# Kernel optimization log

Hardware: AMD Instinct MI355X
Metric: run time of the kernel (lower is better)

## Reference

```python
import jax, jax.numpy as jnp
import numpy as np
import math

D = 1024
H = 16
FF = 4096
BS = 4
N = 1024
NEG_INF = -jnp.inf


def layer_norm(x, g, b, eps=1e-5):
    mu = jnp.mean(x, axis=-1, keepdims=True)
    var = jnp.var(x, axis=-1, keepdims=True)
    return (x - mu) * jax.lax.rsqrt(var + eps) * g + b


def mha(x, kv, Wq, Wk, Wv, g, b, causal):
    bs, n, d = x.shape
    n_kv = kv.shape[1]
    hd = d // H
    q = (x @ Wq).reshape(bs, n, H, hd)
    k = (kv @ Wk).reshape(bs, n_kv, H, hd)
    v = (kv @ Wv).reshape(bs, n_kv, H, hd)
    # scores scaled by 1/sqrt(model_dim) as in the original (not head_dim!)
    scores = jnp.einsum('bihd,bjhd->bhij', q, k) / math.sqrt(d)
    if causal:
        i = jnp.arange(n)[:, None]
        j = jnp.arange(n_kv)[None, :]
        scores = jnp.where(j <= i, scores, NEG_INF)
    probs = jax.nn.softmax(scores, axis=-1)
    ctx = jnp.einsum('bhij,bjhd->bihd', probs, v).reshape(bs, n, d)
    return layer_norm(ctx + x, g, b)


def setup_inputs() -> dict:
    key = jax.random.key(0)
    ks = jax.random.split(key, 20)
    s_attn = 1.0 / math.sqrt(D)
    s_ff1 = 1.0 / math.sqrt(D)
    s_ff2 = 1.0 / math.sqrt(FF)
    return {
        'x': jax.random.normal(ks[0], (BS, N, D), jnp.float32),
        'encoder_out': jax.random.normal(ks[1], (BS, N, D), jnp.float32),
        'Wq1': jax.random.normal(ks[2], (D, D), jnp.float32) * s_attn,
        'Wk1': jax.random.normal(ks[3], (D, D), jnp.float32) * s_attn,
        'Wv1': jax.random.normal(ks[4], (D, D), jnp.float32) * s_attn,
        'g1': jnp.ones((D,), jnp.float32), 'b1': jnp.zeros((D,), jnp.float32),
        'Wq2': jax.random.normal(ks[5], (D, D), jnp.float32) * s_attn,
        'Wk2': jax.random.normal(ks[6], (D, D), jnp.float32) * s_attn,
        'Wv2': jax.random.normal(ks[7], (D, D), jnp.float32) * s_attn,
        'g2': jnp.ones((D,), jnp.float32), 'b2': jnp.zeros((D,), jnp.float32),
        'W_ff1': jax.random.normal(ks[8], (D, FF), jnp.float32) * s_ff1,
        'b_ff1': jnp.zeros((FF,), jnp.float32),
        'W_ff2': jax.random.normal(ks[9], (FF, D), jnp.float32) * s_ff2,
        'b_ff2': jnp.zeros((D,), jnp.float32),
        'g3': jnp.ones((D,), jnp.float32), 'b3': jnp.zeros((D,), jnp.float32),
    }


def reference(x, encoder_out, Wq1, Wk1, Wv1, g1, b1, Wq2, Wk2, Wv2, g2, b2,
              W_ff1, b_ff1, W_ff2, b_ff2, g3, b3):
    # masked (causal) self-attention
    x = mha(x, x, Wq1, Wk1, Wv1, g1, b1, causal=True)
    # cross-attention over encoder output
    x = mha(x, encoder_out, Wq2, Wk2, Wv2, g2, b2, causal=False)
    # feedforward with exact GELU, residual, layernorm
    h = jax.nn.gelu(x @ W_ff1 + b_ff1, approximate=False)
    out = h @ W_ff2 + b_ff2
    return layer_norm(out + x, g3, b3)
```

## Files before the change

### kernel.cpp

```cpp
#include <hip/hip_runtime.h>

typedef unsigned short u16;
typedef short bf16x8 __attribute__((ext_vector_type(8)));
typedef float f32x4 __attribute__((ext_vector_type(4)));
typedef unsigned short u16x8 __attribute__((ext_vector_type(8)));
typedef unsigned short u16x4 __attribute__((ext_vector_type(4)));

__device__ __forceinline__ u16 f2bf(float f) {
  unsigned u = __builtin_bit_cast(unsigned, f);
  u += 0x7fffu + ((u >> 16) & 1u);
  return (u16)(u >> 16);
}
__device__ __forceinline__ float bf2f(u16 v) {
  return __builtin_bit_cast(float, (unsigned)v << 16);
}

__device__ __forceinline__ void gload_lds16(const void* g, void* l) {
  __builtin_amdgcn_global_load_lds(
      (const __attribute__((address_space(1))) unsigned int*)g,
      (__attribute__((address_space(3))) unsigned int*)l, 16, 0, 0);
}

__global__ __launch_bounds__(256) void cast2_bf16_kernel(const float* __restrict__ s0,
                                                         u16* __restrict__ d0,
                                                         const float* __restrict__ s1,
                                                         u16* __restrict__ d1) {
  const float* s = blockIdx.y ? s1 : s0;
  u16* d = blockIdx.y ? d1 : d0;
  const size_t i = (size_t)blockIdx.x * 256 + threadIdx.x;
  const float4 a = ((const float4*)s)[2 * i];
  const float4 b = ((const float4*)s)[2 * i + 1];
  u16x8 o;
  o[0] = f2bf(a.x); o[1] = f2bf(a.y); o[2] = f2bf(a.z); o[3] = f2bf(a.w);
  o[4] = f2bf(b.x); o[5] = f2bf(b.y); o[6] = f2bf(b.z); o[7] = f2bf(b.w);
  ((u16x8*)d)[i] = o;
}

__global__ __launch_bounds__(256) void pack_bt3_kernel(const float* __restrict__ W0,
                                                       const float* __restrict__ W1,
                                                       const float* __restrict__ W2,
                                                       u16* __restrict__ Bt,
                                                       int K, int N) {
  const float* W = blockIdx.z == 0 ? W0 : (blockIdx.z == 1 ? W1 : W2);
  u16* dst0 = Bt + (size_t)blockIdx.z * K * N;
  __shared__ u16 sh[64][72];
  const int n0 = blockIdx.x * 64, k0 = blockIdx.y * 64;
  const int t = threadIdx.x;
  {
    const int kloc = t >> 2, nc = (t & 3) * 16;
    const float* src = W + (size_t)(k0 + kloc) * N + n0 + nc;
#pragma unroll
    for (int i = 0; i < 16; ++i) sh[kloc][nc + i] = f2bf(src[i]);
  }
  __syncthreads();
  {
    const int nloc = t >> 2, kc = (t & 3) * 16;
    u16 tmp[16];
#pragma unroll
    for (int i = 0; i < 16; ++i) tmp[i] = sh[kc + i][nloc];
    u16* dst = dst0 + (size_t)(n0 + nloc) * K + k0 + kc;
    *(u16x8*)dst = *(const u16x8*)tmp;
    *(u16x8*)(dst + 8) = *(const u16x8*)(tmp + 8);
  }
}

__global__ __launch_bounds__(256) void pack_bt_kernel(const float* __restrict__ W,
                                                      u16* __restrict__ Bt,
                                                      int K, int N) {
  __shared__ u16 sh[64][72];
  const int n0 = blockIdx.x * 64, k0 = blockIdx.y * 64;
  const int t = threadIdx.x;
  {
    const int kloc = t >> 2, nc = (t & 3) * 16;
    const float* src = W + (size_t)(k0 + kloc) * N + n0 + nc;
#pragma unroll
    for (int i = 0; i < 16; ++i) sh[kloc][nc + i] = f2bf(src[i]);
  }
  __syncthreads();
  {
    const int nloc = t >> 2, kc = (t & 3) * 16;
    u16 tmp[16];
#pragma unroll
    for (int i = 0; i < 16; ++i) tmp[i] = sh[kc + i][nloc];
    u16* dst = Bt + (size_t)(n0 + nloc) * K + k0 + kc;
    *(u16x8*)dst = *(const u16x8*)tmp;
    *(u16x8*)(dst + 8) = *(const u16x8*)(tmp + 8);
  }
}

template <int EPI, int VOUT>
__global__ __launch_bounds__(512, 4) void gemm_bt(const u16* __restrict__ A,
                                                  const u16* __restrict__ Bt,
                                                  void* __restrict__ Cout,
                                                  const float* __restrict__ bias,
                                                  u16* __restrict__ vt, int voff,
                                                  int M, int N, int K, int lda, int ldb) {
  __shared__ u16 lds[2][2][128 * 64];
  const int tid = threadIdx.x;
  const int lane = tid & 63;
  const int wid = tid >> 6;
  const int wr = wid >> 2;
  const int wc = wid & 3;
  const int g = lane >> 4, cc = lane & 15;
  const int nb = N >> 7;
  const int nwg = gridDim.x;
  const int cpx = nwg >> 3;
  const int bid = (blockIdx.x & 7) * cpx + (blockIdx.x >> 3);
  const int bm = bid / nb, bn = bid % nb;
  const size_t arow0 = (size_t)bm << 7;
  const size_t brow0 = (size_t)bn << 7;
  const size_t koff = (size_t)blockIdx.y * K;

  const u16* ap[2];
  const u16* bp[2];
  int ldst[2];
#pragma unroll
  for (int i = 0; i < 2; ++i) {
    const int tt = i * 512 + tid;
    const int row = tt >> 3;
    const int sc8 = ((tt & 7) ^ (row & 7)) * 8;
    ap[i] = A + (arow0 + row) * lda + koff + sc8;
    bp[i] = Bt + (brow0 + row) * ldb + koff + sc8;
    ldst[i] = (i * 512 + wid * 64) * 8;
  }

  int aoff[4], boff[2];
#pragma unroll
  for (int m = 0; m < 4; ++m) {
    const int rowa = wr * 64 + m * 16 + cc;
    aoff[m] = rowa * 128 + ((g ^ (rowa & 7)) << 4);
  }
#pragma unroll
  for (int n = 0; n < 2; ++n) {
    const int rowb = wc * 32 + n * 16 + cc;
    boff[n] = rowb * 128 + ((g ^ (rowb & 7)) << 4);
  }

  f32x4 acc[4][2] = {};
  const int nk = K >> 6;

#pragma unroll
  for (int i = 0; i < 2; ++i) {
    gload_lds16(ap[i], &lds[0][0][ldst[i]]);
    gload_lds16(bp[i], &lds[0][1][ldst[i]]);
    ap[i] += 64;
    bp[i] += 64;
  }
  __syncthreads();

  int cur = 0;
  for (int kk = 0; kk < nk; ++kk) {
    if (kk + 1 < nk) {
#pragma unroll
      for (int i = 0; i < 2; ++i) {
        gload_lds16(ap[i], &lds[cur ^ 1][0][ldst[i]]);
        gload_lds16(bp[i], &lds[cur ^ 1][1][ldst[i]]);
        ap[i] += 64;
        bp[i] += 64;
      }
    }
    const char* Al = (const char*)&lds[cur][0][0];
    const char* Bl = (const char*)&lds[cur][1][0];
    __builtin_amdgcn_s_setprio(1);
#pragma unroll
    for (int ks = 0; ks < 2; ++ks) {
      const int xr = ks << 6;
      bf16x8 af[4], bfr[2];
#pragma unroll
      for (int m = 0; m < 4; ++m)
        af[m] = *(const bf16x8*)(Al + (aoff[m] ^ xr));
#pragma unroll
      for (int n = 0; n < 2; ++n)
        bfr[n] = *(const bf16x8*)(Bl + (boff[n] ^ xr));
#pragma unroll
      for (int m = 0; m < 4; ++m)
#pragma unroll
        for (int n = 0; n < 2; ++n)
          acc[m][n] = __builtin_amdgcn_mfma_f32_16x16x32_bf16(af[m], bfr[n],
                                                              acc[m][n], 0, 0, 0);
    }
    __builtin_amdgcn_s_setprio(0);
    __syncthreads();
    cur ^= 1;
  }

  const size_t pout = (size_t)blockIdx.y * M * N;
#pragma unroll
  for (int m = 0; m < 4; ++m) {
    const size_t gr0 = arow0 + wr * 64 + m * 16 + (g << 2);
#pragma unroll
    for (int n = 0; n < 2; ++n) {
      const size_t gc = brow0 + wc * 32 + n * 16 + cc;
      if (VOUT && (int)gc >= voff) {
        const int col = (int)gc - voff;
        const int hh = col >> 6, dd = col & 63;
        const int bb = (int)(gr0 >> 10), nn = (int)(gr0 & 1023);
        u16x4 ov;
#pragma unroll
        for (int r = 0; r < 4; ++r) ov[r] = f2bf(acc[m][n][r]);
        *(u16x4*)&vt[(((size_t)(bb * 16 + hh) * 64 + dd) << 10) + nn] = ov;
        continue;
      }
      float bv = 0.f;
      if constexpr (EPI == 1) bv = bias[gc];
#pragma unroll
      for (int r = 0; r < 4; ++r) {
        float v = acc[m][n][r] + bv;
        const size_t idx = (gr0 + r) * (size_t)N + gc;
        if constexpr (EPI == 1) {
          const float u2 = 1.5957691216f * (v + 0.044715f * v * v * v);
          const float e = __expf(u2);
          v = v * e / (e + 1.f);
          ((u16*)Cout)[idx] = f2bf(v);
        } else if constexpr (EPI == 0) {
          ((u16*)Cout)[idx] = f2bf(v);
        } else {
          ((float*)Cout)[pout + idx] = v;
        }
      }
    }
  }
}

template <int CAUSAL>
__global__ __launch_bounds__(256, 6) void attn_kernel(const u16* __restrict__ Qb,
                                                      const u16* __restrict__ Kb,
                                                      const u16* __restrict__ Vt,
                                                      u16* __restrict__ Opart,
                                                      float* __restrict__ lpart,
                                                      int qstride, int kstride) {
  const int qt = blockIdx.x;
  const int bh = blockIdx.y;
  const int z = blockIdx.z;
  const int b = bh >> 4, h = bh & 15;
  const int lane = threadIdx.x & 63;
  const int w = threadIdx.x >> 6;
  const int g = lane >> 4, c = lane & 15;
  const int qbase = qt * 64 + w * 16;

  u16* Op = Opart + (size_t)z * 4096 * 1024;
  float* lp = lpart + (size_t)z * 64 * 1024 + (size_t)bh * 1024;

  int kt0 = z * 8, kt1 = z * 8 + 8;
  if (CAUSAL) kt1 = min(kt1, qt + 1);

  if (kt1 <= kt0) {
#pragma unroll
    for (int r = 0; r < 4; ++r) {
      const int qrow = qbase + g * 4 + r;
      u16x4 zz = {0, 0, 0, 0};
      *(u16x4*)&Op[(size_t)(b * 1024 + qrow) * 1024 + h * 64 + c * 4] = zz;
      if (c == 0) lp[qrow] = 0.f;
    }
    return;
  }

  bf16x8 qf0, qf1;
  {
    const int qrow = qbase + c;
    const u16* qp = Qb + (size_t)(b * 1024 + qrow) * qstride + h * 64 + g * 8;
    qf0 = *(const bf16x8*)qp;
    qf1 = *(const bf16x8*)(qp + 32);
  }

  float l_part[4] = {0.f, 0.f, 0.f, 0.f};
  f32x4 oacc[4] = {};

  __shared__ u16 Kl[64 * 64];
  __shared__ u16 Vl[64 * 64];
  __shared__ u16 Pl[4][16 * 72];
  u16* pw = &Pl[w][0];
  const int tid = threadIdx.x;

  for (int kt = kt0; kt < kt1; ++kt) {
    const int kv0 = kt * 64;
    __syncthreads();
#pragma unroll
    for (int i = 0; i < 2; ++i) {
      const int tt = i * 256 + tid;
      const int row = tt >> 3;
      const int sc = (tt & 7) ^ (row & 7);
      gload_lds16(Kb + (size_t)(b * 1024 + kv0 + row) * kstride + h * 64 + sc * 8,
                  &Kl[(size_t)(i * 256 + w * 64) * 8]);
      gload_lds16(Vt + ((size_t)bh * 64 + row) * 1024 + kv0 + sc * 8,
                  &Vl[(size_t)(i * 256 + w * 64) * 8]);
    }
    __syncthreads();

    f32x4 sacc[4] = {};
#pragma unroll
    for (int t = 0; t < 4; ++t) {
      const int row = t * 16 + c;
      const bf16x8 kf0 = *(const bf16x8*)&Kl[row * 64 + (g ^ (row & 7)) * 8];
      const bf16x8 kf1 = *(const bf16x8*)&Kl[row * 64 + ((4 + g) ^ (row & 7)) * 8];
      sacc[t] = __builtin_amdgcn_mfma_f32_16x16x32_bf16(qf0, kf0, sacc[t], 0, 0, 0);
      sacc[t] = __builtin_amdgcn_mfma_f32_16x16x32_bf16(qf1, kf1, sacc[t], 0, 0, 0);
    }
    const int qr0 = qbase + g * 4;
#pragma unroll
    for (int t = 0; t < 4; ++t) {
      const int kvcol = kv0 + t * 16 + c;
      const int col = t * 16 + c;
#pragma unroll
      for (int r = 0; r < 4; ++r) {
        float p = __expf(sacc[t][r] * 0.03125f);
        if (CAUSAL && kvcol > qr0 + r) p = 0.f;
        l_part[r] += p;
        pw[(g * 4 + r) * 72 + col] = f2bf(p);
      }
    }
#pragma unroll
    for (int ks = 0; ks < 2; ++ks) {
      const bf16x8 pa = *(const bf16x8*)&pw[c * 72 + ks * 32 + g * 8];
#pragma unroll
      for (int t2 = 0; t2 < 4; ++t2) {
        const int row = t2 * 16 + c;
        const bf16x8 vb =
            *(const bf16x8*)&Vl[row * 64 + ((ks * 4 + g) ^ (row & 7)) * 8];
        oacc[t2] = __builtin_amdgcn_mfma_f32_16x16x32_bf16(pa, vb, oacc[t2], 0, 0, 0);
      }
    }
  }
#pragma unroll
  for (int xm = 1; xm < 16; xm <<= 1)
#pragma unroll
    for (int r = 0; r < 4; ++r) l_part[r] += __shfl_xor(l_part[r], xm);
  if (c == 0) {
#pragma unroll
    for (int r = 0; r < 4; ++r) lp[qbase + g * 4 + r] = l_part[r];
  }
#pragma unroll
  for (int t2 = 0; t2 < 4; ++t2) {
    const int d = t2 * 16 + c;
#pragma unroll
    for (int r = 0; r < 4; ++r) {
      const int qrow = qbase + g * 4 + r;
      Op[(size_t)(b * 1024 + qrow) * 1024 + h * 64 + d] = f2bf(oacc[t2][r]);
    }
  }
}

template <int MODE, int RES_BF, int OUT_F>
__global__ __launch_bounds__(256) void add_ln_kernel(const void* __restrict__ a,
                                                     const float* __restrict__ lpart,
                                                     const void* __restrict__ res,
                                                     const float* __restrict__ gam,
                                                     const float* __restrict__ bet,
                                                     float* __restrict__ yf,
                                                     u16* __restrict__ ybf,
                                                     const float* __restrict__ bias) {
  const size_t row = blockIdx.x;
  const int t = threadIdx.x;
  float x[4];
  if constexpr (MODE == 1) {
    const u16* Ob = (const u16*)a;
    const u16x4 p0 = ((const u16x4*)(Ob + row * 1024))[t];
    const u16x4 p1 = ((const u16x4*)(Ob + (size_t)4096 * 1024 + row * 1024))[t];
    const int b = (int)(row >> 10), q = (int)(row & 1023);
    const int h = t >> 4;
    const size_t li = (size_t)(b * 16 + h) * 1024 + q;
    const float inv = 1.f / (lpart[li] + lpart[(size_t)64 * 1024 + li]);
#pragma unroll
    for (int i = 0; i < 4; ++i) x[i] = (bf2f(p0[i]) + bf2f(p1[i])) * inv;
  } else {
    const float* af = (const float*)a;
    float4 av = ((const float4*)(af + row * 1024))[t];
    const float4 a2 = ((const float4*)(af + (size_t)4096 * 1024 + row * 1024))[t];
    const float4 bv2 = ((const float4*)bias)[t];
    x[0] = av.x + a2.x + bv2.x; x[1] = av.y + a2.y + bv2.y;
    x[2] = av.z + a2.z + bv2.z; x[3] = av.w + a2.w + bv2.w;
  }
  if constexpr (RES_BF) {
    const u16x4 rv = ((const u16x4*)((const u16*)res + row * 1024))[t];
#pragma unroll
    for (int i = 0; i < 4; ++i) x[i] += bf2f(rv[i]);
  } else {
    const float4 rv = ((const float4*)((const float*)res + row * 1024))[t];
    x[0] += rv.x; x[1] += rv.y; x[2] += rv.z; x[3] += rv.w;
  }
  float s = x[0] + x[1] + x[2] + x[3];
  float q2 = x[0] * x[0] + x[1] * x[1] + x[2] * x[2] + x[3] * x[3];
#pragma unroll
  for (int m = 1; m < 64; m <<= 1) { s += __shfl_xor(s, m); q2 += __shfl_xor(q2, m); }
  __shared__ float ss[4], sq[4];
  const int w = t >> 6;
  if ((t & 63) == 0) { ss[w] = s; sq[w] = q2; }
  __syncthreads();
  s = ss[0] + ss[1] + ss[2] + ss[3];
  q2 = sq[0] + sq[1] + sq[2] + sq[3];
  const float mu = s * (1.f / 1024.f);
  const float var = q2 * (1.f / 1024.f) - mu * mu;
  const float rstd = rsqrtf(var + 1e-5f);
  const float4 gv = ((const float4*)gam)[t];
  const float4 bv = ((const float4*)bet)[t];
  float y[4];
  y[0] = (x[0] - mu) * rstd * gv.x + bv.x;
  y[1] = (x[1] - mu) * rstd * gv.y + bv.y;
  y[2] = (x[2] - mu) * rstd * gv.z + bv.z;
  y[3] = (x[3] - mu) * rstd * gv.w + bv.w;
  if constexpr (OUT_F) {
    float4 o; o.x = y[0]; o.y = y[1]; o.z = y[2]; o.w = y[3];
    ((float4*)(yf + row * 1024))[t] = o;
  } else {
    u16x4 ob;
    ob[0] = f2bf(y[0]); ob[1] = f2bf(y[1]); ob[2] = f2bf(y[2]); ob[3] = f2bf(y[3]);
    ((u16x4*)(ybf + row * 1024))[t] = ob;
  }
}

extern "C" void kernel_launch(void* const* d_in, const int* in_sizes, int n_in,
                              void* d_out, int out_size, void* d_ws, size_t ws_size,
                              hipStream_t stream) {
  const float* x    = (const float*)d_in[0];
  const float* enc  = (const float*)d_in[1];
  const float* Wq1  = (const float*)d_in[2];
  const float* Wk1  = (const float*)d_in[3];
  const float* Wv1  = (const float*)d_in[4];
  const float* g1   = (const float*)d_in[5];
  const float* b1   = (const float*)d_in[6];
  const float* Wq2  = (const float*)d_in[7];
  const float* Wk2  = (const float*)d_in[8];
  const float* Wv2  = (const float*)d_in[9];
  const float* g2   = (const float*)d_in[10];
  const float* b2   = (const float*)d_in[11];
  const float* Wff1 = (const float*)d_in[12];
  const float* bff1 = (const float*)d_in[13];
  const float* Wff2 = (const float*)d_in[14];
  const float* bff2 = (const float*)d_in[15];
  const float* g3   = (const float*)d_in[16];
  const float* b3   = (const float*)d_in[17];
  float* out = (float*)d_out;

  char* ws = (char*)d_ws;
  const size_t MB = 1024ull * 1024ull;
  u16*   bt  = (u16*)(ws + 0 * MB);
  u16*   big = (u16*)(ws + 8 * MB);
  u16*   vt  = (u16*)(ws + 40 * MB);
  float* ctx = (float*)(ws + 48 * MB);
  float* p1f = (float*)(ws + 64 * MB);
  u16*   abf = (u16*)(ws + 96 * MB);
  u16*   ebf = (u16*)(ws + 104 * MB);
  u16*   opart = (u16*)ctx;
  float* lpart = (float*)bt;
  (void)in_sizes; (void)n_in; (void)out_size; (void)ws_size;

  cast2_bf16_kernel<<<dim3(2048, 2), 256, 0, stream>>>(x, abf, enc, ebf);

  pack_bt3_kernel<<<dim3(16, 16, 3), 256, 0, stream>>>(Wq1, Wk1, Wv1, bt, 1024, 1024);
  gemm_bt<0, 1><<<(4096 / 128) * (3072 / 128), 512, 0, stream>>>(
      abf, bt, big, nullptr, vt, 2048, 4096, 3072, 1024, 1024, 1024);
  attn_kernel<1><<<dim3(16, 64, 2), 256, 0, stream>>>(big, big + 1024, vt, opart, lpart,
                                                      3072, 3072);
  add_ln_kernel<1, 0, 0><<<4096, 256, 0, stream>>>(opart, lpart, x, g1, b1,
                                                   nullptr, abf, nullptr);

  pack_bt3_kernel<<<dim3(16, 16, 3), 256, 0, stream>>>(Wq2, Wk2, Wv2, bt, 1024, 1024);
  u16* q2  = big;
  u16* kv2 = big + (size_t)4096 * 1024;
  gemm_bt<0, 0><<<(4096 / 128) * (1024 / 128), 512, 0, stream>>>(
      abf, bt, q2, nullptr, nullptr, 0, 4096, 1024, 1024, 1024, 1024);
  gemm_bt<0, 1><<<(4096 / 128) * (2048 / 128), 512, 0, stream>>>(
      ebf, bt + (size_t)1024 * 1024, kv2, nullptr, vt, 1024, 4096, 2048, 1024, 1024, 1024);
  attn_kernel<0><<<dim3(16, 64, 2), 256, 0, stream>>>(q2, kv2, vt, opart, lpart, 1024, 2048);
  add_ln_kernel<1, 1, 0><<<4096, 256, 0, stream>>>(opart, lpart, abf, g2, b2,
                                                   nullptr, abf, nullptr);

  pack_bt_kernel<<<dim3(64, 16), 256, 0, stream>>>(Wff1, bt, 1024, 4096);
  gemm_bt<1, 0><<<(4096 / 128) * (4096 / 128), 512, 0, stream>>>(
      abf, bt, big, bff1, nullptr, 0, 4096, 4096, 1024, 1024, 1024);
  pack_bt_kernel<<<dim3(16, 64), 256, 0, stream>>>(Wff2, bt, 4096, 1024);
  gemm_bt<3, 0><<<dim3((4096 / 128) * (1024 / 128), 2), 512, 0, stream>>>(
      big, bt, ctx, nullptr, nullptr, 0, 4096, 1024, 2048, 4096, 4096);
  add_ln_kernel<2, 1, 1><<<4096, 256, 0, stream>>>(ctx, nullptr, abf, g3, b3,
                                                   out, nullptr, bff2);
}
```

Measured before the change: 282.4 us.

## Add 256x256-tile GEMM with 4-stage LDS ring for QKV1 and FF1

Introduces a gemm256 kernel that computes 256x256 output tiles per workgroup with a 4-deep LDS ring of K=32 slices, split prefetches and s_setprio around MFMA blocks, and uses it for the self-attention QKV projection and the first FFN GEMM. Larger tiles raise arithmetic intensity and reduce redundant global/L2 traffic. In exchange, grids shrink to 192 and 256 workgroups, which may underfill the GPU, and occupancy is limited to two workgroups per CU with heavy register use.

```diff
diff --git a/kernel.cpp b/kernel.cpp
--- a/kernel.cpp
+++ b/kernel.cpp
@@ -85,6 +85,144 @@
     u16* dst = Bt + (size_t)(n0 + nloc) * K + k0 + kc;
     *(u16x8*)dst = *(const u16x8*)tmp;
     *(u16x8*)(dst + 8) = *(const u16x8*)(tmp + 8);
+  }
+}
+
+template <int EPI, int VOUT>
+__global__ __launch_bounds__(512, 2) void gemm256(const u16* __restrict__ A,
+                                                  const u16* __restrict__ Bt,
+                                                  void* __restrict__ Cout,
+                                                  const float* __restrict__ bias,
+                                                  u16* __restrict__ vt, int voff,
+                                                  int M, int N, int K, int lda, int ldb) {
+  __shared__ u16 ring[4][2][256 * 32];
+  const int tid = threadIdx.x;
+  const int lane = tid & 63;
+  const int wid = tid >> 6;
+  const int wr = wid >> 2, wc = wid & 3;
+  const int g = lane >> 4, cc = lane & 15;
+  const int nb = N >> 8;
+  const int nwg = gridDim.x, cpx = nwg >> 3;
+  const int bid = (blockIdx.x & 7) * cpx + (blockIdx.x >> 3);
+  const int bm = bid / nb, bn = bid % nb;
+  const size_t arow0 = (size_t)bm << 8;
+  const size_t brow0 = (size_t)bn << 8;
+
+  const int jrow = tid >> 2, jc = tid & 3;
+  const int sch = jc ^ ((jrow >> 1) & 3);
+  const u16* asrc[2] = {A + (arow0 + jrow) * lda + sch * 8,
+                        A + (arow0 + 128 + jrow) * lda + sch * 8};
+  const u16* bsrc[2] = {Bt + (brow0 + jrow) * ldb + sch * 8,
+                        Bt + (brow0 + 128 + jrow) * ldb + sch * 8};
+  const int dstu = wid * 512;
+
+  int aoff[8], boff[4];
+#pragma unroll
+  for (int m = 0; m < 8; ++m) {
+    const int r = wr * 128 + m * 16 + cc;
+    aoff[m] = r * 64 + ((g ^ ((r >> 1) & 3)) << 4);
+  }
+#pragma unroll
+  for (int n = 0; n < 4; ++n) {
+    const int r = wc * 64 + n * 16 + cc;
+    boff[n] = r * 64 + ((g ^ ((r >> 1) & 3)) << 4);
+  }
+
+  f32x4 acc[8][4] = {};
+  const int nk = K >> 5;
+
+#pragma unroll
+  for (int t0 = 0; t0 < 3; ++t0) {
+#pragma unroll
+    for (int h = 0; h < 2; ++h) {
+      gload_lds16(asrc[h] + t0 * 32, &ring[t0][0][h * 4096 + dstu]);
+      gload_lds16(bsrc[h] + t0 * 32, &ring[t0][1][h * 4096 + dstu]);
+    }
+  }
+
+  for (int t = 0; t < nk; ++t) {
+    if (t < nk - 2)       asm volatile("s_waitcnt vmcnt(8)" ::: "memory");
+    else if (t == nk - 2) asm volatile("s_waitcnt vmcnt(4)" ::: "memory");
+    else                  asm volatile("s_waitcnt vmcnt(0)" ::: "memory");
+    __builtin_amdgcn_s_barrier();
+    __builtin_amdgcn_sched_barrier(0);
+    const int s = t & 3;
+    const char* As = (const char*)&ring[s][0][0];
+    const char* Bs = (const char*)&ring[s][1][0];
+    const bool pf = (t + 3 < nk);
+    const int ps = (t + 3) & 3;
+    const size_t kof = (size_t)(t + 3) * 32;
+    if (pf) {
+      gload_lds16(asrc[0] + kof, &ring[ps][0][dstu]);
+      gload_lds16(bsrc[0] + kof, &ring[ps][1][dstu]);
+    }
+    bf16x8 bf4[4];
+#pragma unroll
+    for (int n = 0; n < 4; ++n) bf4[n] = *(const bf16x8*)(Bs + boff[n]);
+    {
+      bf16x8 af[4];
+#pragma unroll
+      for (int m = 0; m < 4; ++m) af[m] = *(const bf16x8*)(As + aoff[m]);
+      __builtin_amdgcn_s_setprio(1);
+#pragma unroll
+      for (int m = 0; m < 4; ++m)
+#pragma unroll
+        for (int n = 0; n < 4; ++n)
+          acc[m][n] = __builtin_amdgcn_mfma_f32_16x16x32_bf16(af[m], bf4[n],
+                                                              acc[m][n], 0, 0, 0);
+      __builtin_amdgcn_s_setprio(0);
+    }
+    if (pf) {
+      gload_lds16(asrc[1] + kof, &ring[ps][0][4096 + dstu]);
+      gload_lds16(bsrc[1] + kof, &ring[ps][1][4096 + dstu]);
+    }
+    {
+      bf16x8 af[4];
+#pragma unroll
+      for (int m = 0; m < 4; ++m) af[m] = *(const bf16x8*)(As + aoff[4 + m]);
+      __builtin_amdgcn_s_setprio(1);
+#pragma unroll
+      for (int m = 0; m < 4; ++m)
+#pragma unroll
+        for (int n = 0; n < 4; ++n)
+          acc[4 + m][n] = __builtin_amdgcn_mfma_f32_16x16x32_bf16(af[m], bf4[n],
+                                                                  acc[4 + m][n], 0, 0, 0);
+      __builtin_amdgcn_s_setprio(0);
+    }
+  }
+
+#pragma unroll
+  for (int m = 0; m < 8; ++m) {
+    const size_t gr0 = arow0 + wr * 128 + m * 16 + (g << 2);
+#pragma unroll
+    for (int n = 0; n < 4; ++n) {
+      const size_t gc = brow0 + wc * 64 + n * 16 + cc;
+      if (VOUT && (int)gc >= voff) {
+        const int col = (int)gc - voff;
+        const int hh = col >> 6, dd = col & 63;
+        const int bb = (int)(gr0 >> 10), nn = (int)(gr0 & 1023);
+        u16x4 ov;
+#pragma unroll
+        for (int r = 0; r < 4; ++r) ov[r] = f2bf(acc[m][n][r]);
+        *(u16x4*)&vt[(((size_t)(bb * 16 + hh) * 64 + dd) << 10) + nn] = ov;
+        continue;
+      }
+      float bv = 0.f;
+      if constexpr (EPI == 1) bv = bias[gc];
+#pragma unroll
+      for (int r = 0; r < 4; ++r) {
+        float v = acc[m][n][r] + bv;
+        const size_t idx = (gr0 + r) * (size_t)N + gc;
+        if constexpr (EPI == 1) {
+          const float u2 = 1.5957691216f * (v + 0.044715f * v * v * v);
+          const float e = __expf(u2);
+          v = v * e / (e + 1.f);
+          ((u16*)Cout)[idx] = f2bf(v);
+        } else {
+          ((u16*)Cout)[idx] = f2bf(v);
+        }
+      }
+    }
   }
 }
 
@@ -437,7 +575,6 @@
   u16*   big = (u16*)(ws + 8 * MB);
   u16*   vt  = (u16*)(ws + 40 * MB);
   float* ctx = (float*)(ws + 48 * MB);
-  float* p1f = (float*)(ws + 64 * MB);
   u16*   abf = (u16*)(ws + 96 * MB);
   u16*   ebf = (u16*)(ws + 104 * MB);
   u16*   opart = (u16*)ctx;
@@ -447,7 +584,7 @@
   cast2_bf16_kernel<<<dim3(2048, 2), 256, 0, stream>>>(x, abf, enc, ebf);
 
   pack_bt3_kernel<<<dim3(16, 16, 3), 256, 0, stream>>>(Wq1, Wk1, Wv1, bt, 1024, 1024);
-  gemm_bt<0, 1><<<(4096 / 128) * (3072 / 128), 512, 0, stream>>>(
+  gemm256<0, 1><<<(4096 / 256) * (3072 / 256), 512, 0, stream>>>(
       abf, bt, big, nullptr, vt, 2048, 4096, 3072, 1024, 1024, 1024);
   attn_kernel<1><<<dim3(16, 64, 2), 256, 0, stream>>>(big, big + 1024, vt, opart, lpart,
                                                       3072, 3072);
@@ -466,7 +603,7 @@
                                                    nullptr, abf, nullptr);
 
   pack_bt_kernel<<<dim3(64, 16), 256, 0, stream>>>(Wff1, bt, 1024, 4096);
-  gemm_bt<1, 0><<<(4096 / 128) * (4096 / 128), 512, 0, stream>>>(
+  gemm256<1, 0><<<(4096 / 256) * (4096 / 256), 512, 0, stream>>>(
       abf, bt, big, bff1, nullptr, 0, 4096, 4096, 1024, 1024, 1024);
   pack_bt_kernel<<<dim3(16, 64), 256, 0, stream>>>(Wff2, bt, 4096, 1024);
   gemm_bt<3, 0><<<dim3((4096 / 128) * (1024 / 128), 2), 512, 0, stream>>>(
```

Result: no change. 283.0 us (+0.2%).
